# Kernel tuning notes

Hardware: AMD Instinct MI355X
Metric: run time of the kernel (lower is better)

Reference implementation:

```python
import jax, jax.numpy as jnp
import numpy as np

HEADS = 8
EPS = 1e-5

def setup_inputs() -> dict:
    key = jax.random.key(0)
    k1, k2, k3 = jax.random.split(key, 3)
    b, c, n = 4, 512, 2048
    x = jax.random.normal(k1, (b, c, n), dtype=jnp.float32)
    g = jnp.ones((c,), dtype=jnp.float32)
    w_qkv = jax.random.normal(k2, (3 * c, c), dtype=jnp.float32) * (1.0 / np.sqrt(c))
    w_out = jax.random.normal(k3, (c, c), dtype=jnp.float32) * (1.0 / np.sqrt(c))
    b_out = jnp.zeros((c,), dtype=jnp.float32)
    return {"x": x, "g": g, "w_qkv": w_qkv, "w_out": w_out, "b_out": b_out}

def reference(x, g, w_qkv, w_out, b_out):
    b, c, n = x.shape
    h = HEADS
    d = c // h
    scale = d ** -0.5
    # channel LayerNorm (biased variance), scale g, no bias
    mean = jnp.mean(x, axis=1, keepdims=True)
    var = jnp.var(x, axis=1, keepdims=True)
    xn = (x - mean) * jax.lax.rsqrt(var + EPS) * g[None, :, None]
    # 1x1 conv == channel matmul: (3c, c) x (b, c, n) -> (b, 3c, n)
    qkv = jnp.einsum('oc,bcn->bon', w_qkv, xn)
    q, k, v = jnp.split(qkv, 3, axis=1)
    # b (h d) n -> b h d n
    q = q.reshape(b, h, d, n) * scale
    k = k.reshape(b, h, d, n)
    v = v.reshape(b, h, d, n)
    sim = jnp.einsum('bhdi,bhdj->bhij', q, k)  # [b,h,n,n]
    attn = jax.nn.softmax(sim, axis=-1)
    out = jnp.einsum('bhij,bhdj->bhid', attn, v)  # [b,h,n,d]
    out = out.transpose(0, 1, 3, 2).reshape(b, h * d, n)  # b (h d) n
    out = jnp.einsum('oc,bcn->bon', w_out, out) + b_out[None, :, None]
    return out
```

## Files before the change

### kernel.cpp

```cpp
#include <hip/hip_runtime.h>
#include <hip/hip_bf16.h>

#define B_ 4
#define C_ 512
#define N_ 2048
#define H_ 8
#define D_ 64
#define O3_ 1536
#define SPLIT 2
#define JTN 16

typedef __bf16 bf16x8 __attribute__((ext_vector_type(8)));
typedef float f32x4 __attribute__((ext_vector_type(4)));
typedef unsigned short ushort_t;

#define QSCALE 0.1803368801111137f

__device__ inline ushort_t f2b(float f) {
    __hip_bfloat16 h = __float2bfloat16(f);
    return *reinterpret_cast<ushort_t*>(&h);
}
__device__ inline float b2f(ushort_t u) {
    unsigned v = ((unsigned)u) << 16;
    return *reinterpret_cast<float*>(&v);
}

__device__ inline void gload16(const ushort_t* g, ushort_t* l) {
    __builtin_amdgcn_global_load_lds(
        (const __attribute__((address_space(1))) unsigned int*)g,
        (__attribute__((address_space(3))) unsigned int*)l, 16, 0, 0);
}


__global__ __launch_bounds__(256) void k_pre(const float* __restrict__ x,
                                             const float* __restrict__ g,
                                             ushort_t* __restrict__ xnT,
                                             const float* __restrict__ wqkv,
                                             const float* __restrict__ wout,
                                             ushort_t* __restrict__ wqkv_b,
                                             ushort_t* __restrict__ wout_b) {
    if (blockIdx.x >= 256) {
        int i = (blockIdx.x - 256) * 256 + threadIdx.x;
        float4 a = reinterpret_cast<const float4*>(wqkv)[i];
        ushort4 o;
        o.x = f2b(a.x); o.y = f2b(a.y); o.z = f2b(a.z); o.w = f2b(a.w);
        reinterpret_cast<ushort4*>(wqkv_b)[i] = o;
        if (i < 65536) {
            float4 c = reinterpret_cast<const float4*>(wout)[i];
            ushort4 oc;
            oc.x = f2b(c.x); oc.y = f2b(c.y); oc.z = f2b(c.z); oc.w = f2b(c.w);
            reinterpret_cast<ushort4*>(wout_b)[i] = oc;
        }
        return;
    }

    int bid = blockIdx.x;
    int b  = bid >> 6;
    int j0 = (bid & 63) * 32;
    int t  = threadIdx.x;

    __shared__ float s_red[8][32];
    __shared__ float s_red2[8][32];
    __shared__ float s_mean[32], s_rstd[32];
    __shared__ float s_g[C_];
    __shared__ __align__(16) ushort_t s_t[32][C_ + 2];

    for (int i = t; i < C_; i += 256) s_g[i] = g[i];

    int jl = t & 31, cg = t >> 5;
    const float* xb = x + (size_t)b * C_ * N_;

    float xv[64];
    float sum = 0.f, sq = 0.f;
#pragma unroll
    for (int i = 0; i < 64; ++i) {
        float v = xb[(size_t)(cg * 64 + i) * N_ + j0 + jl];
        xv[i] = v;
        sum += v; sq += v * v;
    }
    s_red[cg][jl] = sum; s_red2[cg][jl] = sq;
    __syncthreads();
    if (t < 32) {
        float s = 0.f, q = 0.f;
#pragma unroll
        for (int i = 0; i < 8; ++i) { s += s_red[i][t]; q += s_red2[i][t]; }
        float mean = s * (1.0f / C_);
        float var  = q * (1.0f / C_) - mean * mean;
        s_mean[t] = mean;
        s_rstd[t] = rsqrtf(var + 1e-5f);
    }
    __syncthreads();

    float mean = s_mean[jl], rstd = s_rstd[jl];
#pragma unroll
    for (int i = 0; i < 64; ++i) {
        int c = cg * 64 + i;
        s_t[jl][c] = f2b((xv[i] - mean) * rstd * s_g[c]);
    }
    __syncthreads();

    for (int jr = 0; jr < 32; ++jr) {
        unsigned val = *reinterpret_cast<const unsigned*>(&s_t[jr][t * 2]);
        *reinterpret_cast<unsigned*>(
            &xnT[((size_t)(b * N_ + j0 + jr)) * C_ + t * 2]) = val;
    }
}

__global__ __launch_bounds__(256) void k_gemm0(const ushort_t* __restrict__ A,
                                               const ushort_t* __restrict__ Bt,
                                               ushort_t* __restrict__ qT,
                                               ushort_t* __restrict__ kT,
                                               ushort_t* __restrict__ vv) {
    constexpr int K = C_;
    constexpr int NMT = O3_ / 128;
    constexpr int NWG = B_ * NMT * 16;

    int bid  = blockIdx.x;
    int sbid = (bid & 7) * (NWG / 8) + (bid >> 3);
    int b    = sbid / (NMT * 16);
    int rem  = sbid % (NMT * 16);
    int mt0  = (rem / 16) * 128;
    int nt0  = (rem % 16) * 128;

    int t = threadIdx.x;
    int w = t >> 6, lane = t & 63;
    int wm = (w >> 1) * 64, wn = (w & 1) * 64;
    int low = lane & 15, hi = lane >> 4;

    __shared__ __align__(16) ushort_t sA[128][64];
    __shared__ __align__(16) ushort_t sB[128][64];

    const ushort_t* Bb = Bt + (size_t)b * N_ * K;

    int srow = lane >> 3;
    int sseg = (lane & 7) ^ srow;
    const ushort_t* Ag = A  + (size_t)(mt0 + w * 32 + srow) * K + sseg * 8;
    const ushort_t* Bg = Bb + (size_t)(nt0 + w * 32 + srow) * K + sseg * 8;

    f32x4 acc[4][4] = {};

    for (int k0 = 0; k0 < K; k0 += 64) {
#pragma unroll
        for (int i = 0; i < 4; ++i) {
            gload16(Ag + (size_t)(i * 8) * K + k0, &sA[w * 32 + i * 8][0]);
            gload16(Bg + (size_t)(i * 8) * K + k0, &sB[w * 32 + i * 8][0]);
        }
        asm volatile("s_waitcnt vmcnt(0)" ::: "memory");
        __syncthreads();
#pragma unroll
        for (int kk = 0; kk < 64; kk += 32) {
            bf16x8 af[4], bfr[4];
#pragma unroll
            for (int mt = 0; mt < 4; ++mt) {
                int cseg = ((kk >> 3) + hi) ^ (low & 7);
                af[mt] = *reinterpret_cast<const bf16x8*>(
                    &sA[wm + mt * 16 + low][cseg * 8]);
            }
#pragma unroll
            for (int nt = 0; nt < 4; ++nt) {
                int cseg = ((kk >> 3) + hi) ^ (low & 7);
                bfr[nt] = *reinterpret_cast<const bf16x8*>(
                    &sB[wn + nt * 16 + low][cseg * 8]);
            }
#pragma unroll
            for (int mt = 0; mt < 4; ++mt)
#pragma unroll
                for (int nt = 0; nt < 4; ++nt)
                    acc[mt][nt] = __builtin_amdgcn_mfma_f32_16x16x32_bf16(
                        af[mt], bfr[nt], acc[mt][nt], 0, 0, 0);
        }
        __syncthreads();
    }

#pragma unroll
    for (int mt = 0; mt < 4; ++mt)
#pragma unroll
        for (int nt = 0; nt < 4; ++nt) {
            int m0 = mt0 + wm + mt * 16 + hi * 4;
            int j  = nt0 + wn + nt * 16 + low;
            if (m0 < 512) {
                ushort4 pk;
                pk.x = f2b(acc[mt][nt][0] * QSCALE);
                pk.y = f2b(acc[mt][nt][1] * QSCALE);
                pk.z = f2b(acc[mt][nt][2] * QSCALE);
                pk.w = f2b(acc[mt][nt][3] * QSCALE);
                *reinterpret_cast<ushort4*>(
                    &qT[(((size_t)(b * H_ + (m0 >> 6)) * N_) + j) * D_ +
                        (m0 & 63)]) = pk;
            } else if (m0 < 1024) {
                int mm = m0 - 512;
                ushort4 pk;
                pk.x = f2b(acc[mt][nt][0]);
                pk.y = f2b(acc[mt][nt][1]);
                pk.z = f2b(acc[mt][nt][2]);
                pk.w = f2b(acc[mt][nt][3]);
                *reinterpret_cast<ushort4*>(
                    &kT[(((size_t)(b * H_ + (mm >> 6)) * N_) + j) * D_ +
                        (mm & 63)]) = pk;
            } else {
                int mm0 = m0 - 1024;
#pragma unroll
                for (int r = 0; r < 4; ++r)
                    vv[(((size_t)(b * H_ + (mm0 >> 6)) * D_) +
                        ((mm0 & 63) + r)) * N_ + j] = f2b(acc[mt][nt][r]);
            }
        }
}

__global__ __launch_bounds__(512, 4) void k_attn(const ushort_t* __restrict__ qT,
                                                 const ushort_t* __restrict__ kT,
                                                 const ushort_t* __restrict__ vv,
                                                 ushort_t* __restrict__ O0,
                                                 ushort_t* __restrict__ O1,
                                                 float* __restrict__ Lp) {
    int bid  = blockIdx.x;
    int sbid = ((bid & 7) << 6) | (bid >> 3);
    int it256 = sbid & 7;
    int s     = (sbid >> 3) & 1;
    int h     = (sbid >> 4) & 7;
    int b     = sbid >> 7;
    int i0    = it256 * 256;
    int t = threadIdx.x, w = t >> 6, lane = t & 63;
    int low = lane & 15, hi = lane >> 4;

    __shared__ ushort_t sK[2][64][64];
    __shared__ ushort_t sV[2][64][64];
    __shared__ __align__(16) ushort_t sPT[256][72];

    const ushort_t* qb = qT + ((size_t)(b * H_ + h)) * N_ * D_;
    const ushort_t* kb = kT + ((size_t)(b * H_ + h)) * N_ * D_;
    const ushort_t* vb = vv + ((size_t)(b * H_ + h)) * D_ * N_;

    int srow = lane >> 3;
    int sseg = (lane & 7) ^ srow;
    const ushort_t* kg = kb + (size_t)(w * 8 + srow) * D_ + sseg * 8;
    const ushort_t* vg = vb + (size_t)(w * 8 + srow) * N_ + sseg * 8;

    bf16x8 qf[2][2];
#pragma unroll
    for (int mt = 0; mt < 2; ++mt)
#pragma unroll
        for (int kx = 0; kx < 2; ++kx)
            qf[mt][kx] = *reinterpret_cast<const bf16x8*>(
                &qb[(size_t)(i0 + w * 32 + mt * 16 + low) * D_ + kx * 32 + hi * 8]);

    {
        int j0 = s * JTN * 64;
        gload16(kg + (size_t)j0 * D_, &sK[0][w * 8][0]);
        gload16(vg + j0,              &sV[0][w * 8][0]);
    }
    asm volatile("s_waitcnt vmcnt(0)" ::: "memory");
    __syncthreads();

    f32x4 oacc[2][4] = {};
    float lp0 = 0.f, lp1 = 0.f;
    int sw = (low & 7) * 8;

    int buf = 0;
    for (int jj = 0; jj < JTN; ++jj) {
        int j0c = (s * JTN + jj) * 64;

        if (jj + 1 < JTN) {
            int j0n = j0c + 64;
            gload16(kg + (size_t)j0n * D_, &sK[buf ^ 1][w * 8][0]);
            gload16(vg + j0n,              &sV[buf ^ 1][w * 8][0]);
        }

        f32x4 sacc[2][4] = {};
#pragma unroll
        for (int kx = 0; kx < 2; ++kx) {
            bf16x8 kfx[4];
#pragma unroll
            for (int nt = 0; nt < 4; ++nt)
                kfx[nt] = *reinterpret_cast<const bf16x8*>(
                    &sK[buf][nt * 16 + low][((kx * 4 + hi) * 8) ^ sw]);
#pragma unroll
            for (int mt = 0; mt < 2; ++mt)
#pragma unroll
                for (int nt = 0; nt < 4; ++nt)
                    sacc[mt][nt] = __builtin_amdgcn_mfma_f32_16x16x32_bf16(
                        kfx[nt], qf[mt][kx], sacc[mt][nt], 0, 0, 0);
        }

        bf16x8 vf[2][4];
#pragma unroll
        for (int kx = 0; kx < 2; ++kx)
#pragma unroll
            for (int dt = 0; dt < 4; ++dt)
                vf[kx][dt] = *reinterpret_cast<const bf16x8*>(
                    &sV[buf][dt * 16 + low][((kx * 4 + hi) * 8) ^ sw]);

#pragma unroll
        for (int mt = 0; mt < 2; ++mt) {
            int qrow = w * 32 + mt * 16 + low;
#pragma unroll
            for (int nt = 0; nt < 4; ++nt) {
                float p0 = __builtin_amdgcn_exp2f(sacc[mt][nt][0]);
                float p1 = __builtin_amdgcn_exp2f(sacc[mt][nt][1]);
                float p2 = __builtin_amdgcn_exp2f(sacc[mt][nt][2]);
                float p3 = __builtin_amdgcn_exp2f(sacc[mt][nt][3]);
                if (mt == 0) lp0 += (p0 + p1) + (p2 + p3);
                else         lp1 += (p0 + p1) + (p2 + p3);
                ushort4 pk;
                pk.x = f2b(p0); pk.y = f2b(p1); pk.z = f2b(p2); pk.w = f2b(p3);
                *reinterpret_cast<ushort4*>(&sPT[qrow][nt * 16 + hi * 4]) = pk;
            }
        }

#pragma unroll
        for (int kx = 0; kx < 2; ++kx) {
            bf16x8 ap0 = *reinterpret_cast<const bf16x8*>(
                &sPT[w * 32 + low][kx * 32 + hi * 8]);
            bf16x8 ap1 = *reinterpret_cast<const bf16x8*>(
                &sPT[w * 32 + 16 + low][kx * 32 + hi * 8]);
#pragma unroll
            for (int dt = 0; dt < 4; ++dt) {
                oacc[0][dt] = __builtin_amdgcn_mfma_f32_16x16x32_bf16(
                    ap0, vf[kx][dt], oacc[0][dt], 0, 0, 0);
                oacc[1][dt] = __builtin_amdgcn_mfma_f32_16x16x32_bf16(
                    ap1, vf[kx][dt], oacc[1][dt], 0, 0, 0);
            }
        }

        asm volatile("s_waitcnt vmcnt(0)" ::: "memory");
        __syncthreads();
        buf ^= 1;
    }

    lp0 += __shfl_xor(lp0, 16); lp0 += __shfl_xor(lp0, 32);
    lp1 += __shfl_xor(lp1, 16); lp1 += __shfl_xor(lp1, 32);

    float* lrow = Lp + ((size_t)((s * B_ + b) * H_ + h)) * N_ + i0 + w * 32;
    if (lane < 16) {
        lrow[low]      = lp0;
        lrow[16 + low] = lp1;
    }

    ushort_t* op = (s == 0 ? O0 : O1) +
                   ((size_t)(b * N_ + i0 + w * 32)) * C_ + h * D_;
#pragma unroll
    for (int mt = 0; mt < 2; ++mt)
#pragma unroll
        for (int dt = 0; dt < 4; ++dt)
#pragma unroll
            for (int r = 0; r < 4; ++r)
                op[(size_t)(mt * 16 + hi * 4 + r) * C_ + dt * 16 + low] =
                    f2b(oacc[mt][dt][r]);
}

__global__ __launch_bounds__(256) void k_gemm1(const ushort_t* __restrict__ A,
                                               const ushort_t* __restrict__ O0,
                                               const ushort_t* __restrict__ O1,
                                               const float* __restrict__ Lp,
                                               float* __restrict__ out,
                                               const float* __restrict__ b_out) {
    constexpr int K = C_;
    constexpr int NMT = C_ / 64;
    constexpr int NWG = B_ * NMT * 16;

    int bid  = blockIdx.x;
    int sbid = (bid & 7) * (NWG / 8) + (bid >> 3);
    int b    = sbid / (NMT * 16);
    int rem  = sbid % (NMT * 16);
    int mt0  = (rem / 16) * 64;
    int nt0  = (rem % 16) * 128;

    int t = threadIdx.x;
    int w = t >> 6, lane = t & 63;
    int wm = (w >> 1) * 32, wn = (w & 1) * 64;
    int low = lane & 15, hi = lane >> 4;

    __shared__ __align__(16) ushort_t sA[64][64];
    __shared__ __align__(16) ushort_t sB[128][64];

    int srow = lane >> 3;
    int sseg = (lane & 7) ^ srow;
    int wseg = lane & 7;
    const ushort_t* Ag = A + (size_t)(mt0 + w * 16 + srow) * K + sseg * 8;

    f32x4 acc[2][4] = {};

    for (int k0 = 0; k0 < K; k0 += 64) {
        int h = k0 >> 6;
#pragma unroll
        for (int i = 0; i < 2; ++i)
            gload16(Ag + (size_t)(i * 8) * K + k0, &sA[w * 16 + i * 8][0]);

#pragma unroll
        for (int it = 0; it < 4; ++it) {
            int jr = w * 32 + it * 8 + srow;
            int j  = nt0 + jr;
            size_t obase = ((size_t)(b * N_ + j)) * C_ + k0 + sseg * 8;
            ushort4 a0 = *reinterpret_cast<const ushort4*>(&O0[obase]);
            ushort4 a1 = *reinterpret_cast<const ushort4*>(&O0[obase + 4]);
            ushort4 c0 = *reinterpret_cast<const ushort4*>(&O1[obase]);
            ushort4 c1 = *reinterpret_cast<const ushort4*>(&O1[obase + 4]);
            float l = Lp[((size_t)(b * H_ + h)) * N_ + j] +
                      Lp[((size_t)((B_ + b) * H_ + h)) * N_ + j];
            float linv = 1.0f / l;
            ushort4 o0, o1;
            o0.x = f2b((b2f(a0.x) + b2f(c0.x)) * linv);
            o0.y = f2b((b2f(a0.y) + b2f(c0.y)) * linv);
            o0.z = f2b((b2f(a0.z) + b2f(c0.z)) * linv);
            o0.w = f2b((b2f(a0.w) + b2f(c0.w)) * linv);
            o1.x = f2b((b2f(a1.x) + b2f(c1.x)) * linv);
            o1.y = f2b((b2f(a1.y) + b2f(c1.y)) * linv);
            o1.z = f2b((b2f(a1.z) + b2f(c1.z)) * linv);
            o1.w = f2b((b2f(a1.w) + b2f(c1.w)) * linv);
            *reinterpret_cast<ushort4*>(&sB[jr][wseg * 8])     = o0;
            *reinterpret_cast<ushort4*>(&sB[jr][wseg * 8 + 4]) = o1;
        }

        asm volatile("s_waitcnt vmcnt(0)" ::: "memory");
        __syncthreads();
#pragma unroll
        for (int kk = 0; kk < 64; kk += 32) {
            bf16x8 af[2], bfr[4];
#pragma unroll
            for (int mt = 0; mt < 2; ++mt) {
                int cseg = ((kk >> 3) + hi) ^ (low & 7);
                af[mt] = *reinterpret_cast<const bf16x8*>(
                    &sA[wm + mt * 16 + low][cseg * 8]);
            }
#pragma unroll
            for (int nt = 0; nt < 4; ++nt) {
                int cseg = ((kk >> 3) + hi) ^ (low & 7);
                bfr[nt] = *reinterpret_cast<const bf16x8*>(
                    &sB[wn + nt * 16 + low][cseg * 8]);
            }
#pragma unroll
            for (int mt = 0; mt < 2; ++mt)
#pragma unroll
                for (int nt = 0; nt < 4; ++nt)
                    acc[mt][nt] = __builtin_amdgcn_mfma_f32_16x16x32_bf16(
                        af[mt], bfr[nt], acc[mt][nt], 0, 0, 0);
        }
        __syncthreads();
    }

#pragma unroll
    for (int mt = 0; mt < 2; ++mt)
#pragma unroll
        for (int nt = 0; nt < 4; ++nt) {
            int m0 = mt0 + wm + mt * 16 + hi * 4;
            int j  = nt0 + wn + nt * 16 + low;
#pragma unroll
            for (int r = 0; r < 4; ++r)
                out[((size_t)(b * C_ + m0 + r)) * N_ + j] =
                    acc[mt][nt][r] + b_out[m0 + r];
        }
}

extern "C" void kernel_launch(void* const* d_in, const int* in_sizes, int n_in,
                              void* d_out, int out_size, void* d_ws, size_t ws_size,
                              hipStream_t stream) {
    const float* x    = (const float*)d_in[0];
    const float* g    = (const float*)d_in[1];
    const float* wqkv = (const float*)d_in[2];
    const float* wout = (const float*)d_in[3];
    const float* bout = (const float*)d_in[4];
    float* out = (float*)d_out;

    char* ws = (char*)d_ws;
    ushort_t* xnT    = (ushort_t*)(ws);
    ushort_t* qT     = (ushort_t*)(ws + (size_t)8  * 1024 * 1024);
    ushort_t* kT     = (ushort_t*)(ws + (size_t)16 * 1024 * 1024);
    ushort_t* vv     = (ushort_t*)(ws + (size_t)24 * 1024 * 1024);
    ushort_t* O0     = (ushort_t*)(ws + (size_t)32 * 1024 * 1024);
    ushort_t* wqkv_b = (ushort_t*)(ws + (size_t)40 * 1024 * 1024);
    ushort_t* wout_b = (ushort_t*)(ws + (size_t)42 * 1024 * 1024);
    float*    Lp     = (float*)   (ws + (size_t)43 * 1024 * 1024);

    k_pre<<<dim3(1024), dim3(256), 0, stream>>>(
        x, g, xnT, wqkv, wout, wqkv_b, wout_b);
    k_gemm0<<<dim3(B_ * (O3_ / 128) * (N_ / 128)), dim3(256), 0, stream>>>(
        wqkv_b, xnT, qT, kT, vv);
    k_attn<<<dim3(B_ * H_ * (N_ / 256) * SPLIT), dim3(512), 0, stream>>>(
        qT, kT, vv, O0, xnT, Lp);
    k_gemm1<<<dim3(B_ * (C_ / 64) * (N_ / 128)), dim3(256), 0, stream>>>(
        wout_b, O0, xnT, Lp, out, bout);
}
```

Before: 92.87 us.

## Triple-buffer K/V tiles and halve the P staging buffer in attention

Moves the K/V shared-memory staging from double to triple buffering, prefetching two tiles ahead and waiting with vmcnt(2), so global loads have more time to overlap compute. The P tile is now written and consumed in two 32-column halves, which shrinks sPT from 72 to 40 columns and offsets the extra LDS used by the third K/V buffer. The trade-offs are more in-flight loads and a tighter dependency between the P writes and the PV MFMA within each half. Because of the wait placement, the loop relies on the ordering of the gload16 instructions.

```diff
diff --git a/kernel.cpp b/kernel.cpp
--- a/kernel.cpp
+++ b/kernel.cpp
@@ -223,9 +223,9 @@
     int t = threadIdx.x, w = t >> 6, lane = t & 63;
     int low = lane & 15, hi = lane >> 4;
 
-    __shared__ ushort_t sK[2][64][64];
-    __shared__ ushort_t sV[2][64][64];
-    __shared__ __align__(16) ushort_t sPT[256][72];
+    __shared__ ushort_t sK[3][64][64];
+    __shared__ ushort_t sV[3][64][64];
+    __shared__ __align__(16) ushort_t sPT[256][40];
 
     const ushort_t* qb = qT + ((size_t)(b * H_ + h)) * N_ * D_;
     const ushort_t* kb = kT + ((size_t)(b * H_ + h)) * N_ * D_;
@@ -246,24 +246,26 @@
 
     {
         int j0 = s * JTN * 64;
-        gload16(kg + (size_t)j0 * D_, &sK[0][w * 8][0]);
-        gload16(vg + j0,              &sV[0][w * 8][0]);
-    }
-    asm volatile("s_waitcnt vmcnt(0)" ::: "memory");
+        gload16(kg + (size_t)j0 * D_,        &sK[0][w * 8][0]);
+        gload16(vg + j0,                     &sV[0][w * 8][0]);
+        gload16(kg + (size_t)(j0 + 64) * D_, &sK[1][w * 8][0]);
+        gload16(vg + (j0 + 64),              &sV[1][w * 8][0]);
+    }
+    asm volatile("s_waitcnt vmcnt(2)" ::: "memory");
     __syncthreads();
 
     f32x4 oacc[2][4] = {};
     float lp0 = 0.f, lp1 = 0.f;
     int sw = (low & 7) * 8;
 
-    int buf = 0;
+    int bcur = 0;
     for (int jj = 0; jj < JTN; ++jj) {
-        int j0c = (s * JTN + jj) * 64;
-
-        if (jj + 1 < JTN) {
-            int j0n = j0c + 64;
-            gload16(kg + (size_t)j0n * D_, &sK[buf ^ 1][w * 8][0]);
-            gload16(vg + j0n,              &sV[buf ^ 1][w * 8][0]);
+        int bnext = bcur + 2; if (bnext >= 3) bnext -= 3;
+        bool pf = (jj + 2 < JTN);
+        if (pf) {
+            int j0n = (s * JTN + jj + 2) * 64;
+            gload16(kg + (size_t)j0n * D_, &sK[bnext][w * 8][0]);
+            gload16(vg + j0n,              &sV[bnext][w * 8][0]);
         }
 
         f32x4 sacc[2][4] = {};
@@ -273,7 +275,7 @@
 #pragma unroll
             for (int nt = 0; nt < 4; ++nt)
                 kfx[nt] = *reinterpret_cast<const bf16x8*>(
-                    &sK[buf][nt * 16 + low][((kx * 4 + hi) * 8) ^ sw]);
+                    &sK[bcur][nt * 16 + low][((kx * 4 + hi) * 8) ^ sw]);
 #pragma unroll
             for (int mt = 0; mt < 2; ++mt)
 #pragma unroll
@@ -288,43 +290,46 @@
 #pragma unroll
             for (int dt = 0; dt < 4; ++dt)
                 vf[kx][dt] = *reinterpret_cast<const bf16x8*>(
-                    &sV[buf][dt * 16 + low][((kx * 4 + hi) * 8) ^ sw]);
-
-#pragma unroll
-        for (int mt = 0; mt < 2; ++mt) {
-            int qrow = w * 32 + mt * 16 + low;
-#pragma unroll
-            for (int nt = 0; nt < 4; ++nt) {
-                float p0 = __builtin_amdgcn_exp2f(sacc[mt][nt][0]);
-                float p1 = __builtin_amdgcn_exp2f(sacc[mt][nt][1]);
-                float p2 = __builtin_amdgcn_exp2f(sacc[mt][nt][2]);
-                float p3 = __builtin_amdgcn_exp2f(sacc[mt][nt][3]);
-                if (mt == 0) lp0 += (p0 + p1) + (p2 + p3);
-                else         lp1 += (p0 + p1) + (p2 + p3);
-                ushort4 pk;
-                pk.x = f2b(p0); pk.y = f2b(p1); pk.z = f2b(p2); pk.w = f2b(p3);
-                *reinterpret_cast<ushort4*>(&sPT[qrow][nt * 16 + hi * 4]) = pk;
-            }
-        }
-
-#pragma unroll
-        for (int kx = 0; kx < 2; ++kx) {
+                    &sV[bcur][dt * 16 + low][((kx * 4 + hi) * 8) ^ sw]);
+
+#pragma unroll
+        for (int hx = 0; hx < 2; ++hx) {
+#pragma unroll
+            for (int mt = 0; mt < 2; ++mt) {
+                int qrow = w * 32 + mt * 16 + low;
+#pragma unroll
+                for (int nt2 = 0; nt2 < 2; ++nt2) {
+                    int nt = hx * 2 + nt2;
+                    float p0 = __builtin_amdgcn_exp2f(sacc[mt][nt][0]);
+                    float p1 = __builtin_amdgcn_exp2f(sacc[mt][nt][1]);
+                    float p2 = __builtin_amdgcn_exp2f(sacc[mt][nt][2]);
+                    float p3 = __builtin_amdgcn_exp2f(sacc[mt][nt][3]);
+                    if (mt == 0) lp0 += (p0 + p1) + (p2 + p3);
+                    else         lp1 += (p0 + p1) + (p2 + p3);
+                    ushort4 pk;
+                    pk.x = f2b(p0); pk.y = f2b(p1);
+                    pk.z = f2b(p2); pk.w = f2b(p3);
+                    *reinterpret_cast<ushort4*>(
+                        &sPT[qrow][nt2 * 16 + hi * 4]) = pk;
+                }
+            }
             bf16x8 ap0 = *reinterpret_cast<const bf16x8*>(
-                &sPT[w * 32 + low][kx * 32 + hi * 8]);
+                &sPT[w * 32 + low][hi * 8]);
             bf16x8 ap1 = *reinterpret_cast<const bf16x8*>(
-                &sPT[w * 32 + 16 + low][kx * 32 + hi * 8]);
+                &sPT[w * 32 + 16 + low][hi * 8]);
 #pragma unroll
             for (int dt = 0; dt < 4; ++dt) {
                 oacc[0][dt] = __builtin_amdgcn_mfma_f32_16x16x32_bf16(
-                    ap0, vf[kx][dt], oacc[0][dt], 0, 0, 0);
+                    ap0, vf[hx][dt], oacc[0][dt], 0, 0, 0);
                 oacc[1][dt] = __builtin_amdgcn_mfma_f32_16x16x32_bf16(
-                    ap1, vf[kx][dt], oacc[1][dt], 0, 0, 0);
-            }
-        }
-
-        asm volatile("s_waitcnt vmcnt(0)" ::: "memory");
+                    ap1, vf[hx][dt], oacc[1][dt], 0, 0, 0);
+            }
+        }
+
+        if (pf) asm volatile("s_waitcnt vmcnt(2)" ::: "memory");
+        else    asm volatile("s_waitcnt vmcnt(0)" ::: "memory");
         __syncthreads();
-        buf ^= 1;
+        bcur += 1; if (bcur >= 3) bcur -= 3;
     }
 
     lp0 += __shfl_xor(lp0, 16); lp0 += __shfl_xor(lp0, 32);
```

After: 92.55 us. No clear change (-0.3%).

## Split attention key range four ways and merge partials in output GEMM

Applied to the files above, without the earlier changes.

Raises the key-dimension split in the attention kernel from 2 to 4. This doubles the number of workgroups, each handling 8 key tiles instead of 16. The probability staging buffer is cut to half width by writing and consuming P in two 32-column halves per tile, which lowers LDS use per block. The output projection GEMM now reads and sums four bf16 partial outputs and four row-sum partials. The aim is better CU occupancy and load balance, paid for with extra global write and read traffic for the two new partial buffers and more workspace.

```diff
diff --git a/kernel.cpp b/kernel.cpp
--- a/kernel.cpp
+++ b/kernel.cpp
@@ -7,8 +7,8 @@
 #define H_ 8
 #define D_ 64
 #define O3_ 1536
-#define SPLIT 2
-#define JTN 16
+#define SPLIT 4
+#define JT4 8
 
 typedef __bf16 bf16x8 __attribute__((ext_vector_type(8)));
 typedef float f32x4 __attribute__((ext_vector_type(4)));
@@ -212,20 +212,22 @@
                                                  const ushort_t* __restrict__ vv,
                                                  ushort_t* __restrict__ O0,
                                                  ushort_t* __restrict__ O1,
+                                                 ushort_t* __restrict__ O2,
+                                                 ushort_t* __restrict__ O3,
                                                  float* __restrict__ Lp) {
     int bid  = blockIdx.x;
-    int sbid = ((bid & 7) << 6) | (bid >> 3);
+    int sbid = ((bid & 7) << 7) | (bid >> 3);
     int it256 = sbid & 7;
-    int s     = (sbid >> 3) & 1;
-    int h     = (sbid >> 4) & 7;
-    int b     = sbid >> 7;
+    int s     = (sbid >> 3) & 3;
+    int h     = (sbid >> 5) & 7;
+    int b     = sbid >> 8;
     int i0    = it256 * 256;
     int t = threadIdx.x, w = t >> 6, lane = t & 63;
     int low = lane & 15, hi = lane >> 4;
 
     __shared__ ushort_t sK[2][64][64];
     __shared__ ushort_t sV[2][64][64];
-    __shared__ __align__(16) ushort_t sPT[256][72];
+    __shared__ __align__(16) ushort_t sPT[256][40];
 
     const ushort_t* qb = qT + ((size_t)(b * H_ + h)) * N_ * D_;
     const ushort_t* kb = kT + ((size_t)(b * H_ + h)) * N_ * D_;
@@ -245,7 +247,7 @@
                 &qb[(size_t)(i0 + w * 32 + mt * 16 + low) * D_ + kx * 32 + hi * 8]);
 
     {
-        int j0 = s * JTN * 64;
+        int j0 = s * JT4 * 64;
         gload16(kg + (size_t)j0 * D_, &sK[0][w * 8][0]);
         gload16(vg + j0,              &sV[0][w * 8][0]);
     }
@@ -257,11 +259,9 @@
     int sw = (low & 7) * 8;
 
     int buf = 0;
-    for (int jj = 0; jj < JTN; ++jj) {
-        int j0c = (s * JTN + jj) * 64;
-
-        if (jj + 1 < JTN) {
-            int j0n = j0c + 64;
+    for (int jj = 0; jj < JT4; ++jj) {
+        if (jj + 1 < JT4) {
+            int j0n = (s * JT4 + jj + 1) * 64;
             gload16(kg + (size_t)j0n * D_, &sK[buf ^ 1][w * 8][0]);
             gload16(vg + j0n,              &sV[buf ^ 1][w * 8][0]);
         }
@@ -291,34 +291,36 @@
                     &sV[buf][dt * 16 + low][((kx * 4 + hi) * 8) ^ sw]);
 
 #pragma unroll
-        for (int mt = 0; mt < 2; ++mt) {
-            int qrow = w * 32 + mt * 16 + low;
-#pragma unroll
-            for (int nt = 0; nt < 4; ++nt) {
-                float p0 = __builtin_amdgcn_exp2f(sacc[mt][nt][0]);
-                float p1 = __builtin_amdgcn_exp2f(sacc[mt][nt][1]);
-                float p2 = __builtin_amdgcn_exp2f(sacc[mt][nt][2]);
-                float p3 = __builtin_amdgcn_exp2f(sacc[mt][nt][3]);
-                if (mt == 0) lp0 += (p0 + p1) + (p2 + p3);
-                else         lp1 += (p0 + p1) + (p2 + p3);
-                ushort4 pk;
-                pk.x = f2b(p0); pk.y = f2b(p1); pk.z = f2b(p2); pk.w = f2b(p3);
-                *reinterpret_cast<ushort4*>(&sPT[qrow][nt * 16 + hi * 4]) = pk;
-            }
-        }
-
-#pragma unroll
-        for (int kx = 0; kx < 2; ++kx) {
+        for (int hx = 0; hx < 2; ++hx) {
+#pragma unroll
+            for (int mt = 0; mt < 2; ++mt) {
+                int qrow = w * 32 + mt * 16 + low;
+#pragma unroll
+                for (int nt2 = 0; nt2 < 2; ++nt2) {
+                    int nt = hx * 2 + nt2;
+                    float p0 = __builtin_amdgcn_exp2f(sacc[mt][nt][0]);
+                    float p1 = __builtin_amdgcn_exp2f(sacc[mt][nt][1]);
+                    float p2 = __builtin_amdgcn_exp2f(sacc[mt][nt][2]);
+                    float p3 = __builtin_amdgcn_exp2f(sacc[mt][nt][3]);
+                    if (mt == 0) lp0 += (p0 + p1) + (p2 + p3);
+                    else         lp1 += (p0 + p1) + (p2 + p3);
+                    ushort4 pk;
+                    pk.x = f2b(p0); pk.y = f2b(p1);
+                    pk.z = f2b(p2); pk.w = f2b(p3);
+                    *reinterpret_cast<ushort4*>(
+                        &sPT[qrow][nt2 * 16 + hi * 4]) = pk;
+                }
+            }
             bf16x8 ap0 = *reinterpret_cast<const bf16x8*>(
-                &sPT[w * 32 + low][kx * 32 + hi * 8]);
+                &sPT[w * 32 + low][hi * 8]);
             bf16x8 ap1 = *reinterpret_cast<const bf16x8*>(
-                &sPT[w * 32 + 16 + low][kx * 32 + hi * 8]);
+                &sPT[w * 32 + 16 + low][hi * 8]);
 #pragma unroll
             for (int dt = 0; dt < 4; ++dt) {
                 oacc[0][dt] = __builtin_amdgcn_mfma_f32_16x16x32_bf16(
-                    ap0, vf[kx][dt], oacc[0][dt], 0, 0, 0);
+                    ap0, vf[hx][dt], oacc[0][dt], 0, 0, 0);
                 oacc[1][dt] = __builtin_amdgcn_mfma_f32_16x16x32_bf16(
-                    ap1, vf[kx][dt], oacc[1][dt], 0, 0, 0);
+                    ap1, vf[hx][dt], oacc[1][dt], 0, 0, 0);
             }
         }
 
@@ -336,7 +338,7 @@
         lrow[16 + low] = lp1;
     }
 
-    ushort_t* op = (s == 0 ? O0 : O1) +
+    ushort_t* op = (s == 0 ? O0 : s == 1 ? O1 : s == 2 ? O2 : O3) +
                    ((size_t)(b * N_ + i0 + w * 32)) * C_ + h * D_;
 #pragma unroll
     for (int mt = 0; mt < 2; ++mt)
@@ -351,6 +353,8 @@
 __global__ __launch_bounds__(256) void k_gemm1(const ushort_t* __restrict__ A,
                                                const ushort_t* __restrict__ O0,
                                                const ushort_t* __restrict__ O1,
+                                               const ushort_t* __restrict__ O2,
+                                               const ushort_t* __restrict__ O3,
                                                const float* __restrict__ Lp,
                                                float* __restrict__ out,
                                                const float* __restrict__ b_out) {
@@ -395,18 +399,24 @@
             ushort4 a1 = *reinterpret_cast<const ushort4*>(&O0[obase + 4]);
             ushort4 c0 = *reinterpret_cast<const ushort4*>(&O1[obase]);
             ushort4 c1 = *reinterpret_cast<const ushort4*>(&O1[obase + 4]);
+            ushort4 d0 = *reinterpret_cast<const ushort4*>(&O2[obase]);
+            ushort4 d1 = *reinterpret_cast<const ushort4*>(&O2[obase + 4]);
+            ushort4 e0 = *reinterpret_cast<const ushort4*>(&O3[obase]);
+            ushort4 e1 = *reinterpret_cast<const ushort4*>(&O3[obase + 4]);
             float l = Lp[((size_t)(b * H_ + h)) * N_ + j] +
-                      Lp[((size_t)((B_ + b) * H_ + h)) * N_ + j];
+                      Lp[((size_t)((B_ + b) * H_ + h)) * N_ + j] +
+                      Lp[((size_t)((2 * B_ + b) * H_ + h)) * N_ + j] +
+                      Lp[((size_t)((3 * B_ + b) * H_ + h)) * N_ + j];
             float linv = 1.0f / l;
             ushort4 o0, o1;
-            o0.x = f2b((b2f(a0.x) + b2f(c0.x)) * linv);
-            o0.y = f2b((b2f(a0.y) + b2f(c0.y)) * linv);
-            o0.z = f2b((b2f(a0.z) + b2f(c0.z)) * linv);
-            o0.w = f2b((b2f(a0.w) + b2f(c0.w)) * linv);
-            o1.x = f2b((b2f(a1.x) + b2f(c1.x)) * linv);
-            o1.y = f2b((b2f(a1.y) + b2f(c1.y)) * linv);
-            o1.z = f2b((b2f(a1.z) + b2f(c1.z)) * linv);
-            o1.w = f2b((b2f(a1.w) + b2f(c1.w)) * linv);
+            o0.x = f2b((b2f(a0.x) + b2f(c0.x) + b2f(d0.x) + b2f(e0.x)) * linv);
+            o0.y = f2b((b2f(a0.y) + b2f(c0.y) + b2f(d0.y) + b2f(e0.y)) * linv);
+            o0.z = f2b((b2f(a0.z) + b2f(c0.z) + b2f(d0.z) + b2f(e0.z)) * linv);
+            o0.w = f2b((b2f(a0.w) + b2f(c0.w) + b2f(d0.w) + b2f(e0.w)) * linv);
+            o1.x = f2b((b2f(a1.x) + b2f(c1.x) + b2f(d1.x) + b2f(e1.x)) * linv);
+            o1.y = f2b((b2f(a1.y) + b2f(c1.y) + b2f(d1.y) + b2f(e1.y)) * linv);
+            o1.z = f2b((b2f(a1.z) + b2f(c1.z) + b2f(d1.z) + b2f(e1.z)) * linv);
+            o1.w = f2b((b2f(a1.w) + b2f(c1.w) + b2f(d1.w) + b2f(e1.w)) * linv);
             *reinterpret_cast<ushort4*>(&sB[jr][wseg * 8])     = o0;
             *reinterpret_cast<ushort4*>(&sB[jr][wseg * 8 + 4]) = o1;
         }
@@ -470,13 +480,15 @@
     ushort_t* wqkv_b = (ushort_t*)(ws + (size_t)40 * 1024 * 1024);
     ushort_t* wout_b = (ushort_t*)(ws + (size_t)42 * 1024 * 1024);
     float*    Lp     = (float*)   (ws + (size_t)43 * 1024 * 1024);
+    ushort_t* O2     = (ushort_t*)(ws + (size_t)44 * 1024 * 1024);
+    ushort_t* O3     = (ushort_t*)(ws + (size_t)52 * 1024 * 1024);
 
     k_pre<<<dim3(1024), dim3(256), 0, stream>>>(
         x, g, xnT, wqkv, wout, wqkv_b, wout_b);
     k_gemm0<<<dim3(B_ * (O3_ / 128) * (N_ / 128)), dim3(256), 0, stream>>>(
         wqkv_b, xnT, qT, kT, vv);
     k_attn<<<dim3(B_ * H_ * (N_ / 256) * SPLIT), dim3(512), 0, stream>>>(
-        qT, kT, vv, O0, xnT, Lp);
+        qT, kT, vv, O0, xnT, O2, O3, Lp);
     k_gemm1<<<dim3(B_ * (C_ / 64) * (N_ / 128)), dim3(256), 0, stream>>>(
-        wout_b, O0, xnT, Lp, out, bout);
-}
+        wout_b, O0, xnT, O2, O3, Lp, out, bout);
+}
```

Result: slower. 107.8 us (+16.1%).
